# Optimization experiments

Measured on AMD Instinct MI355X. Metric: run time of the kernel, lower is better.

The kernel has to match this reference:

```python
import jax, jax.numpy as jnp
import numpy as np

E = 2048   # embed_dim
H = 16     # num query heads
D = E // H # head_dim = 128
B = 2
S = 2048


def setup_inputs() -> dict:
    key = jax.random.key(0)
    ks = jax.random.split(key, 12)
    sc = 0.02
    return {
        "input": jax.random.normal(ks[0], (B, S, E), jnp.float32),
        "kv": jax.random.normal(ks[1], (B, S, E), jnp.float32),
        "Wq": jax.random.normal(ks[2], (E, E), jnp.float32) * sc,
        "bq": jnp.zeros((E,), jnp.float32),
        "Wk": jax.random.normal(ks[3], (D, E), jnp.float32) * sc,
        "bk": jnp.zeros((D,), jnp.float32),
        "Wv": jax.random.normal(ks[4], (D, E), jnp.float32) * sc,
        "bv": jnp.zeros((D,), jnp.float32),
        "Wo": jax.random.normal(ks[5], (E, E), jnp.float32) * sc,
        "bo": jnp.zeros((E,), jnp.float32),
        "expanding_context": 0,
    }


def reference(input, kv, Wq, bq, Wk, bk, Wv, bv, Wo, bo, expanding_context):
    b, s, _ = input.shape
    # projections (torch Linear: x @ W.T + b)
    q = (input @ Wq.T + bq).reshape(b, s, H, D).transpose(0, 2, 1, 3)  # [B,H,S,D]
    k = kv @ Wk.T + bk  # [B,S,D] single KV head
    v = kv @ Wv.T + bv  # [B,S,D]
    # scores with single KV head broadcast across query heads
    scores = jnp.einsum('bhsd,btd->bhst', q, k) / jnp.sqrt(jnp.float32(D))
    causal = jnp.triu(jnp.ones((s, s), bool), k=1)  # True above diagonal
    scores = jnp.where(causal[None, None], jnp.float32(-jnp.inf), scores)
    attn = jax.nn.softmax(scores, axis=-1)
    out = jnp.einsum('bhst,btd->bhsd', attn, v)  # [B,H,S,D]
    out = out.transpose(0, 2, 1, 3).reshape(b, s, E)
    return out @ Wo.T + bo
```

## Files before the change

### kernel.cpp

```cpp
#include <hip/hip_runtime.h>

#define B_  2
#define S_  2048
#define E_  2048
#define H_  16
#define D_  128
#define BS_ (B_*S_)

typedef __bf16 bf16_t;
typedef __bf16 bf16x8 __attribute__((ext_vector_type(8)));
typedef __bf16 bf16x4 __attribute__((ext_vector_type(4)));
typedef float  f32x4  __attribute__((ext_vector_type(4)));

#define QSCALE 0.1275174131003543f

__device__ __forceinline__ void gld16(const bf16_t* g, bf16_t* l) {
    __builtin_amdgcn_global_load_lds(
        (const __attribute__((address_space(1))) void*)g,
        (__attribute__((address_space(3))) void*)l,
        16, 0, 0);
}

__global__ void cvt_all(const float* __restrict__ s0, const float* __restrict__ s1,
                        const float* __restrict__ s2, const float* __restrict__ s3,
                        const float* __restrict__ s4, const float* __restrict__ s5,
                        bf16_t* d0, bf16_t* d1, bf16_t* d2,
                        bf16_t* d3, bf16_t* d4, bf16_t* d5)
{
    long i = ((long)blockIdx.x * blockDim.x + threadIdx.x) * 4;
    const float* s; bf16_t* d;
    if      (i <  8388608) { s = s0; d = d0; }
    else if (i < 16777216) { s = s1; d = d1; i -=  8388608; }
    else if (i < 20971520) { s = s2; d = d2; i -= 16777216; }
    else if (i < 21233664) { s = s3; d = d3; i -= 20971520; }
    else if (i < 21495808) { s = s4; d = d4; i -= 21233664; }
    else                   { s = s5; d = d5; i -= 21495808; }
    float4 v = *(const float4*)(s + i);
    bf16x4 o;
    o[0] = (bf16_t)v.x; o[1] = (bf16_t)v.y; o[2] = (bf16_t)v.z; o[3] = (bf16_t)v.w;
    *(bf16x4*)(d + i) = o;
}

__device__ __forceinline__ void gemm_tile(
    const bf16_t* __restrict__ A, const bf16_t* __restrict__ W,
    const float* __restrict__ biasA, const float* __restrict__ biasB,
    float* __restrict__ Cf, bf16_t* __restrict__ Cb,
    int N, int K, float scale, int m0, int n0,
    bf16_t* As, bf16_t* Bs)
{
    const int tid  = threadIdx.x;
    const int wave = tid >> 6, lane = tid & 63;
    const int wm = wave >> 1, wn = wave & 1;
    const int lrow = lane & 15, quad = lane >> 4;
    const int r8 = lane >> 3, c8 = (lane & 7) << 3;

    f32x4 acc[4][4] = {};

    for (int k0 = 0; k0 < K; k0 += 64) {
        __syncthreads();
#pragma unroll
        for (int j = 0; j < 4; ++j) {
            int base = (wave * 4 + j) * 8;
            gld16(A + (size_t)(m0 + base + r8) * K + k0 + c8, &As[base * 64]);
            gld16(W + (size_t)(n0 + base + r8) * K + k0 + c8, &Bs[base * 64]);
        }
        __syncthreads();
#pragma unroll
        for (int ks = 0; ks < 2; ++ks) {
            bf16x8 af[4], bfr[4];
#pragma unroll
            for (int mt = 0; mt < 4; ++mt)
                af[mt] = *(const bf16x8*)&As[(wm * 64 + mt * 16 + lrow) * 64 + ks * 32 + quad * 8];
#pragma unroll
            for (int nt = 0; nt < 4; ++nt)
                bfr[nt] = *(const bf16x8*)&Bs[(wn * 64 + nt * 16 + lrow) * 64 + ks * 32 + quad * 8];
#pragma unroll
            for (int mt = 0; mt < 4; ++mt)
#pragma unroll
                for (int nt = 0; nt < 4; ++nt)
                    acc[mt][nt] = __builtin_amdgcn_mfma_f32_16x16x32_bf16(
                        af[mt], bfr[nt], acc[mt][nt], 0, 0, 0);
        }
    }

#pragma unroll
    for (int mt = 0; mt < 4; ++mt) {
#pragma unroll
        for (int nt = 0; nt < 4; ++nt) {
            int col = n0 + wn * 64 + nt * 16 + lrow;
            const float* bp = biasA; int ci = col;
            if (biasB && col >= 128) { bp = biasB; ci = col - 128; }
            float bv = bp[ci];
#pragma unroll
            for (int r = 0; r < 4; ++r) {
                int row = m0 + wm * 64 + mt * 16 + quad * 4 + r;
                float v = (acc[mt][nt][r] + bv) * scale;
                if (Cf) Cf[(size_t)row * N + col] = v;
                else    Cb[(size_t)row * N + col] = (bf16_t)v;
            }
        }
    }
}

__global__ __launch_bounds__(256) void gemm_qkv(
    const bf16_t* __restrict__ xb, const bf16_t* __restrict__ kvb,
    const bf16_t* __restrict__ Wq, const bf16_t* __restrict__ Wkv,
    const float* __restrict__ bq, const float* __restrict__ bk,
    const float* __restrict__ bv,
    bf16_t* __restrict__ Qb, bf16_t* __restrict__ KVb)
{
    __shared__ __align__(16) bf16_t As[128 * 64];
    __shared__ __align__(16) bf16_t Bs[128 * 64];
    const int m0 = blockIdx.y * 128;
    if (blockIdx.x < 16) {
        gemm_tile(xb, Wq, bq, nullptr, nullptr, Qb, E_, E_, QSCALE,
                  m0, blockIdx.x * 128, As, Bs);
    } else {
        gemm_tile(kvb, Wkv, bk, bv, nullptr, KVb, 256, E_, 1.0f,
                  m0, (blockIdx.x - 16) * 128, As, Bs);
    }
}

__global__ __launch_bounds__(256) void gemm_o(
    const bf16_t* __restrict__ A, const bf16_t* __restrict__ W,
    const float* __restrict__ bias, float* __restrict__ Cf)
{
    __shared__ __align__(16) bf16_t As[128 * 64];
    __shared__ __align__(16) bf16_t Bs[128 * 64];
    gemm_tile(A, W, bias, nullptr, Cf, nullptr, E_, E_, 1.0f,
              blockIdx.y * 128, blockIdx.x * 128, As, Bs);
}

__global__ __launch_bounds__(512, 4) void mqa_attn(
    const bf16_t* __restrict__ Q, const bf16_t* __restrict__ KV,
    bf16_t* __restrict__ O)
{
    __shared__ __align__(16) bf16_t Kt[64][136];
    __shared__ __align__(16) bf16_t Vt[128][72];
    __shared__ __align__(16) bf16_t Pl[8][16][72];

    const int bx = blockIdx.x, h = blockIdx.y, b = blockIdx.z;
    const int qb = b ? bx : (15 - bx);
    const int tid = threadIdx.x, wave = tid >> 6, lane = tid & 63;
    const int lrow = lane & 15, quad = lane >> 4;
    const int q0 = qb * 128 + wave * 16;

    const bf16_t* kvp = KV + (size_t)(b * S_) * 256;

    bf16x8 qf[4];
    {
        const bf16_t* qp = Q + ((size_t)(b * S_ + q0 + lrow)) * E_ + h * D_ + quad * 8;
#pragma unroll
        for (int ks = 0; ks < 4; ++ks) qf[ks] = *(const bf16x8*)(qp + ks * 32);
    }

    f32x4 oacc[8] = {};
    float rs[4] = {0.f, 0.f, 0.f, 0.f};

    const int ntiles = 2 * qb + 2;
    bf16x8 kreg[2], vreg[2];

#pragma unroll
    for (int i = 0; i < 2; ++i) {
        int c = tid + 512 * i;
        kreg[i] = *(const bf16x8*)(kvp + (size_t)(c >> 4) * 256 + ((c & 15) << 3));
        vreg[i] = *(const bf16x8*)(kvp + (size_t)(c & 63) * 256 + 128 + ((c >> 6) << 3));
    }

    for (int kt = 0; kt < ntiles; ++kt) {
        const int k_base = kt * 64;
        __syncthreads();
#pragma unroll
        for (int i = 0; i < 2; ++i) {
            int c = tid + 512 * i;
            *(bf16x8*)&Kt[c >> 4][(c & 15) << 3] = kreg[i];
            int n = c & 63, d0 = (c >> 6) << 3;
#pragma unroll
            for (int j = 0; j < 8; ++j) Vt[d0 + j][n] = vreg[i][j];
        }
        __syncthreads();
        if (kt + 1 < ntiles) {
            const int nb = (kt + 1) * 64;
#pragma unroll
            for (int i = 0; i < 2; ++i) {
                int c = tid + 512 * i;
                kreg[i] = *(const bf16x8*)(kvp + (size_t)(nb + (c >> 4)) * 256 + ((c & 15) << 3));
                vreg[i] = *(const bf16x8*)(kvp + (size_t)(nb + (c & 63)) * 256 + 128 + ((c >> 6) << 3));
            }
        }

        if (k_base <= q0 + 15) {
            f32x4 sc[4] = {};
#pragma unroll
            for (int ks = 0; ks < 4; ++ks) {
                bf16x8 a = qf[ks];
#pragma unroll
                for (int c = 0; c < 4; ++c) {
                    bf16x8 kb = *(const bf16x8*)&Kt[c * 16 + lrow][ks * 32 + quad * 8];
                    sc[c] = __builtin_amdgcn_mfma_f32_16x16x32_bf16(a, kb, sc[c], 0, 0, 0);
                }
            }
            const bool diag = (k_base + 63 > q0);
#pragma unroll
            for (int c = 0; c < 4; ++c) {
#pragma unroll
                for (int r = 0; r < 4; ++r) {
                    float s = sc[c][r];
                    if (diag) {
                        int kj = k_base + c * 16 + lrow;
                        int qi = q0 + quad * 4 + r;
                        if (kj > qi) s = -1e30f;
                    }
                    float p = exp2f(fminf(s, 110.f));
                    rs[r] += p;
                    Pl[wave][quad * 4 + r][c * 16 + lrow] = (bf16_t)p;
                }
            }
#pragma unroll
            for (int ks = 0; ks < 2; ++ks) {
                bf16x8 ap = *(const bf16x8*)&Pl[wave][lrow][ks * 32 + quad * 8];
#pragma unroll
                for (int dt = 0; dt < 8; ++dt) {
                    bf16x8 bv = *(const bf16x8*)&Vt[dt * 16 + lrow][ks * 32 + quad * 8];
                    oacc[dt] = __builtin_amdgcn_mfma_f32_16x16x32_bf16(ap, bv, oacc[dt], 0, 0, 0);
                }
            }
        }
    }

#pragma unroll
    for (int off = 8; off >= 1; off >>= 1)
#pragma unroll
        for (int r = 0; r < 4; ++r) rs[r] += __shfl_xor(rs[r], off, 16);
#pragma unroll
    for (int r = 0; r < 4; ++r) {
        float inv = 1.0f / rs[r];
        int row = q0 + quad * 4 + r;
#pragma unroll
        for (int dt = 0; dt < 8; ++dt)
            O[((size_t)(b * S_ + row)) * E_ + h * D_ + dt * 16 + lrow] =
                (bf16_t)(oacc[dt][r] * inv);
    }
}

extern "C" void kernel_launch(void* const* d_in, const int* in_sizes, int n_in,
                              void* d_out, int out_size, void* d_ws, size_t ws_size,
                              hipStream_t stream)
{
    const float* x   = (const float*)d_in[0];
    const float* kv  = (const float*)d_in[1];
    const float* Wq  = (const float*)d_in[2];
    const float* bq  = (const float*)d_in[3];
    const float* Wk  = (const float*)d_in[4];
    const float* bk  = (const float*)d_in[5];
    const float* Wv  = (const float*)d_in[6];
    const float* bv  = (const float*)d_in[7];
    const float* Wo  = (const float*)d_in[8];
    const float* bo  = (const float*)d_in[9];
    float* out = (float*)d_out;

    bf16_t* p    = (bf16_t*)d_ws;
    bf16_t* xb   = p;  p += (size_t)BS_ * E_;
    bf16_t* kvb  = p;  p += (size_t)BS_ * E_;
    bf16_t* Wqb  = p;  p += (size_t)E_ * E_;
    bf16_t* Wkvb = p;  p += (size_t)2 * D_ * E_;
    bf16_t* Wob  = p;  p += (size_t)E_ * E_;
    bf16_t* Qb   = p;  p += (size_t)BS_ * E_;
    bf16_t* KVb  = p;  p += (size_t)BS_ * 256;
    bf16_t* Ob   = p;  p += (size_t)BS_ * E_;

    cvt_all<<<dim3(25088), dim3(256), 0, stream>>>(
        x, kv, Wq, Wk, Wv, Wo,
        xb, kvb, Wqb, Wkvb, Wkvb + (size_t)D_ * E_, Wob);

    gemm_qkv<<<dim3(18, BS_ / 128), 256, 0, stream>>>(
        xb, kvb, Wqb, Wkvb, bq, bk, bv, Qb, KVb);

    mqa_attn<<<dim3(S_ / 128, H_, B_), 512, 0, stream>>>(Qb, KVb, Ob);

    gemm_o<<<dim3(E_ / 128, BS_ / 128), 256, 0, stream>>>(Ob, Wob, bo, out);
}
```

Baseline: 365.7 us.

## Fuse fp32 activation conversion into QKV GEMM with register-staged double buffering

Stops converting the x and kv activations to bf16 in a separate pass. The QKV GEMM now reads fp32 activations directly and converts them while staging tiles into LDS, and only the weights are still pre-converted. The GEMM tile loop is rewritten from global_load_lds with two barriers per step to a register-prefetched, double-buffered LDS pipeline with one barrier per step. This saves a full activation read/write pass, but doubles LDS per block and raises register pressure, and the QKV GEMM now reads fp32 A tiles, so it moves twice the bytes for them.

```diff
diff --git a/kernel.cpp b/kernel.cpp
--- a/kernel.cpp
+++ b/kernel.cpp
@@ -14,66 +14,110 @@
 
 #define QSCALE 0.1275174131003543f
 
-__device__ __forceinline__ void gld16(const bf16_t* g, bf16_t* l) {
-    __builtin_amdgcn_global_load_lds(
-        (const __attribute__((address_space(1))) void*)g,
-        (__attribute__((address_space(3))) void*)l,
-        16, 0, 0);
-}
-
-__global__ void cvt_all(const float* __restrict__ s0, const float* __restrict__ s1,
-                        const float* __restrict__ s2, const float* __restrict__ s3,
-                        const float* __restrict__ s4, const float* __restrict__ s5,
-                        bf16_t* d0, bf16_t* d1, bf16_t* d2,
-                        bf16_t* d3, bf16_t* d4, bf16_t* d5)
+__global__ void cvt_w(const float* __restrict__ s0, const float* __restrict__ s1,
+                      const float* __restrict__ s2, const float* __restrict__ s3,
+                      bf16_t* d0, bf16_t* d1, bf16_t* d2, bf16_t* d3)
 {
     long i = ((long)blockIdx.x * blockDim.x + threadIdx.x) * 4;
     const float* s; bf16_t* d;
-    if      (i <  8388608) { s = s0; d = d0; }
-    else if (i < 16777216) { s = s1; d = d1; i -=  8388608; }
-    else if (i < 20971520) { s = s2; d = d2; i -= 16777216; }
-    else if (i < 21233664) { s = s3; d = d3; i -= 20971520; }
-    else if (i < 21495808) { s = s4; d = d4; i -= 21233664; }
-    else                   { s = s5; d = d5; i -= 21495808; }
+    if      (i < 4194304) { s = s0; d = d0; }
+    else if (i < 4456448) { s = s1; d = d1; i -= 4194304; }
+    else if (i < 4718592) { s = s2; d = d2; i -= 4456448; }
+    else                  { s = s3; d = d3; i -= 4718592; }
     float4 v = *(const float4*)(s + i);
     bf16x4 o;
     o[0] = (bf16_t)v.x; o[1] = (bf16_t)v.y; o[2] = (bf16_t)v.z; o[3] = (bf16_t)v.w;
     *(bf16x4*)(d + i) = o;
 }
 
-__device__ __forceinline__ void gemm_tile(
-    const bf16_t* __restrict__ A, const bf16_t* __restrict__ W,
-    const float* __restrict__ biasA, const float* __restrict__ biasB,
+template<bool AF32>
+__device__ __forceinline__ void gemm_tile_db(
+    const void* Ap, const bf16_t* __restrict__ W,
+    const float* __restrict__ bias,
     float* __restrict__ Cf, bf16_t* __restrict__ Cb,
-    int N, int K, float scale, int m0, int n0,
+    int N, int K, float scale, int m0, int w_n0, int c_n0,
     bf16_t* As, bf16_t* Bs)
 {
     const int tid  = threadIdx.x;
     const int wave = tid >> 6, lane = tid & 63;
     const int wm = wave >> 1, wn = wave & 1;
     const int lrow = lane & 15, quad = lane >> 4;
-    const int r8 = lane >> 3, c8 = (lane & 7) << 3;
+
+    const float*  Af = (const float*)Ap;
+    const bf16_t* Ab = (const bf16_t*)Ap;
+
+    float4 arf[8];
+    uint4  arb[4];
+    uint4  brb[4];
+
+    auto loadA = [&](int k0) {
+        if constexpr (AF32) {
+#pragma unroll
+            for (int j = 0; j < 8; ++j) {
+                int c = tid + 256 * j, row = c >> 4, col = (c & 15) << 2;
+                arf[j] = *(const float4*)(Af + (size_t)(m0 + row) * K + k0 + col);
+            }
+        } else {
+#pragma unroll
+            for (int j = 0; j < 4; ++j) {
+                int c = tid + 256 * j, row = c >> 3, col = (c & 7) << 3;
+                arb[j] = *(const uint4*)(Ab + (size_t)(m0 + row) * K + k0 + col);
+            }
+        }
+    };
+    auto loadB = [&](int k0) {
+#pragma unroll
+        for (int j = 0; j < 4; ++j) {
+            int c = tid + 256 * j, row = c >> 3, col = (c & 7) << 3;
+            brb[j] = *(const uint4*)(W + (size_t)(w_n0 + row) * K + k0 + col);
+        }
+    };
+    auto storeA = [&](bf16_t* dst) {
+        if constexpr (AF32) {
+#pragma unroll
+            for (int j = 0; j < 8; ++j) {
+                int c = tid + 256 * j, row = c >> 4, col = (c & 15) << 2;
+                bf16x4 o;
+                o[0] = (bf16_t)arf[j].x; o[1] = (bf16_t)arf[j].y;
+                o[2] = (bf16_t)arf[j].z; o[3] = (bf16_t)arf[j].w;
+                *(bf16x4*)&dst[row * 64 + col] = o;
+            }
+        } else {
+#pragma unroll
+            for (int j = 0; j < 4; ++j) {
+                int c = tid + 256 * j, row = c >> 3, col = (c & 7) << 3;
+                *(uint4*)&dst[row * 64 + col] = arb[j];
+            }
+        }
+    };
+    auto storeB = [&](bf16_t* dst) {
+#pragma unroll
+        for (int j = 0; j < 4; ++j) {
+            int c = tid + 256 * j, row = c >> 3, col = (c & 7) << 3;
+            *(uint4*)&dst[row * 64 + col] = brb[j];
+        }
+    };
 
     f32x4 acc[4][4] = {};
 
+    loadA(0); loadB(0);
+    storeA(As); storeB(Bs);
+    loadA(64); loadB(64);
+
+    int cur = 0;
     for (int k0 = 0; k0 < K; k0 += 64) {
         __syncthreads();
-#pragma unroll
-        for (int j = 0; j < 4; ++j) {
-            int base = (wave * 4 + j) * 8;
-            gld16(A + (size_t)(m0 + base + r8) * K + k0 + c8, &As[base * 64]);
-            gld16(W + (size_t)(n0 + base + r8) * K + k0 + c8, &Bs[base * 64]);
-        }
-        __syncthreads();
+        const bf16_t* Ac = As + cur * 8192;
+        const bf16_t* Bc = Bs + cur * 8192;
 #pragma unroll
         for (int ks = 0; ks < 2; ++ks) {
             bf16x8 af[4], bfr[4];
 #pragma unroll
             for (int mt = 0; mt < 4; ++mt)
-                af[mt] = *(const bf16x8*)&As[(wm * 64 + mt * 16 + lrow) * 64 + ks * 32 + quad * 8];
+                af[mt] = *(const bf16x8*)&Ac[(wm * 64 + mt * 16 + lrow) * 64 + ks * 32 + quad * 8];
 #pragma unroll
             for (int nt = 0; nt < 4; ++nt)
-                bfr[nt] = *(const bf16x8*)&Bs[(wn * 64 + nt * 16 + lrow) * 64 + ks * 32 + quad * 8];
+                bfr[nt] = *(const bf16x8*)&Bc[(wn * 64 + nt * 16 + lrow) * 64 + ks * 32 + quad * 8];
 #pragma unroll
             for (int mt = 0; mt < 4; ++mt)
 #pragma unroll
@@ -81,20 +125,25 @@
                     acc[mt][nt] = __builtin_amdgcn_mfma_f32_16x16x32_bf16(
                         af[mt], bfr[nt], acc[mt][nt], 0, 0, 0);
         }
+        if (k0 + 64 < K) {
+            storeA(As + (cur ^ 1) * 8192);
+            storeB(Bs + (cur ^ 1) * 8192);
+            if (k0 + 128 < K) { loadA(k0 + 128); loadB(k0 + 128); }
+        }
+        cur ^= 1;
     }
 
 #pragma unroll
     for (int mt = 0; mt < 4; ++mt) {
 #pragma unroll
         for (int nt = 0; nt < 4; ++nt) {
-            int col = n0 + wn * 64 + nt * 16 + lrow;
-            const float* bp = biasA; int ci = col;
-            if (biasB && col >= 128) { bp = biasB; ci = col - 128; }
-            float bv = bp[ci];
+            int nn = wn * 64 + nt * 16 + lrow;
+            float bvv = bias[w_n0 + nn];
+            int col = c_n0 + nn;
 #pragma unroll
             for (int r = 0; r < 4; ++r) {
                 int row = m0 + wm * 64 + mt * 16 + quad * 4 + r;
-                float v = (acc[mt][nt][r] + bv) * scale;
+                float v = (acc[mt][nt][r] + bvv) * scale;
                 if (Cf) Cf[(size_t)row * N + col] = v;
                 else    Cb[(size_t)row * N + col] = (bf16_t)v;
             }
@@ -102,33 +151,36 @@
     }
 }
 
-__global__ __launch_bounds__(256) void gemm_qkv(
-    const bf16_t* __restrict__ xb, const bf16_t* __restrict__ kvb,
-    const bf16_t* __restrict__ Wq, const bf16_t* __restrict__ Wkv,
+__global__ __launch_bounds__(256, 2) void gemm_qkv(
+    const float* __restrict__ x, const float* __restrict__ kv,
+    const bf16_t* __restrict__ Wq, const bf16_t* __restrict__ Wk,
+    const bf16_t* __restrict__ Wv,
     const float* __restrict__ bq, const float* __restrict__ bk,
     const float* __restrict__ bv,
     bf16_t* __restrict__ Qb, bf16_t* __restrict__ KVb)
 {
-    __shared__ __align__(16) bf16_t As[128 * 64];
-    __shared__ __align__(16) bf16_t Bs[128 * 64];
+    __shared__ __align__(16) bf16_t As[2 * 8192];
+    __shared__ __align__(16) bf16_t Bs[2 * 8192];
     const int m0 = blockIdx.y * 128;
     if (blockIdx.x < 16) {
-        gemm_tile(xb, Wq, bq, nullptr, nullptr, Qb, E_, E_, QSCALE,
-                  m0, blockIdx.x * 128, As, Bs);
+        int n0 = blockIdx.x * 128;
+        gemm_tile_db<true>(x, Wq, bq, nullptr, Qb, E_, E_, QSCALE, m0, n0, n0, As, Bs);
+    } else if (blockIdx.x == 16) {
+        gemm_tile_db<true>(kv, Wk, bk, nullptr, KVb, 256, E_, 1.0f, m0, 0, 0, As, Bs);
     } else {
-        gemm_tile(kvb, Wkv, bk, bv, nullptr, KVb, 256, E_, 1.0f,
-                  m0, (blockIdx.x - 16) * 128, As, Bs);
-    }
-}
-
-__global__ __launch_bounds__(256) void gemm_o(
+        gemm_tile_db<true>(kv, Wv, bv, nullptr, KVb, 256, E_, 1.0f, m0, 0, 128, As, Bs);
+    }
+}
+
+__global__ __launch_bounds__(256, 2) void gemm_o(
     const bf16_t* __restrict__ A, const bf16_t* __restrict__ W,
     const float* __restrict__ bias, float* __restrict__ Cf)
 {
-    __shared__ __align__(16) bf16_t As[128 * 64];
-    __shared__ __align__(16) bf16_t Bs[128 * 64];
-    gemm_tile(A, W, bias, nullptr, Cf, nullptr, E_, E_, 1.0f,
-              blockIdx.y * 128, blockIdx.x * 128, As, Bs);
+    __shared__ __align__(16) bf16_t As[2 * 8192];
+    __shared__ __align__(16) bf16_t Bs[2 * 8192];
+    int n0 = blockIdx.x * 128;
+    gemm_tile_db<false>(A, W, bias, Cf, nullptr, E_, E_, 1.0f,
+                        blockIdx.y * 128, n0, n0, As, Bs);
 }
 
 __global__ __launch_bounds__(512, 4) void mqa_attn(
@@ -260,21 +312,19 @@
     float* out = (float*)d_out;
 
     bf16_t* p    = (bf16_t*)d_ws;
-    bf16_t* xb   = p;  p += (size_t)BS_ * E_;
-    bf16_t* kvb  = p;  p += (size_t)BS_ * E_;
     bf16_t* Wqb  = p;  p += (size_t)E_ * E_;
-    bf16_t* Wkvb = p;  p += (size_t)2 * D_ * E_;
+    bf16_t* Wkb  = p;  p += (size_t)D_ * E_;
+    bf16_t* Wvb  = p;  p += (size_t)D_ * E_;
     bf16_t* Wob  = p;  p += (size_t)E_ * E_;
     bf16_t* Qb   = p;  p += (size_t)BS_ * E_;
     bf16_t* KVb  = p;  p += (size_t)BS_ * 256;
     bf16_t* Ob   = p;  p += (size_t)BS_ * E_;
 
-    cvt_all<<<dim3(25088), dim3(256), 0, stream>>>(
-        x, kv, Wq, Wk, Wv, Wo,
-        xb, kvb, Wqb, Wkvb, Wkvb + (size_t)D_ * E_, Wob);
+    cvt_w<<<dim3(8704), dim3(256), 0, stream>>>(
+        Wq, Wk, Wv, Wo, Wqb, Wkb, Wvb, Wob);
 
     gemm_qkv<<<dim3(18, BS_ / 128), 256, 0, stream>>>(
-        xb, kvb, Wqb, Wkvb, bq, bk, bv, Qb, KVb);
+        x, kv, Wqb, Wkb, Wvb, bq, bk, bv, Qb, KVb);
 
     mqa_attn<<<dim3(S_ / 128, H_, B_), 512, 0, stream>>>(Qb, KVb, Ob);
 
```

Measured after the change: 495.0 us. +35.4%, slower.

## Split-K the Q and output projection GEMMs with fp32 atomic accumulation

Applied to the files above, without the earlier changes.

The Q projection and output projection GEMMs are split into two halves along K via a third grid dimension, with partial results combined by fp32 atomicAdd into zeroed buffers. The intent is to double the block count for these 512-tile GEMMs and fill more compute units. Q is now stored as fp32 and scaled and converted to bf16 inside the attention kernel, and the input buffer is reused for the attention output. This costs extra memsets, atomic traffic, doubled Q storage bandwidth, and an accumulation order that is no longer deterministic.

```diff
diff --git a/kernel.cpp b/kernel.cpp
--- a/kernel.cpp
+++ b/kernel.cpp
@@ -41,11 +41,12 @@
     *(bf16x4*)(d + i) = o;
 }
 
-__device__ __forceinline__ void gemm_tile(
+template<int EP>
+__device__ __forceinline__ void gemm_tile_sk(
     const bf16_t* __restrict__ A, const bf16_t* __restrict__ W,
     const float* __restrict__ biasA, const float* __restrict__ biasB,
     float* __restrict__ Cf, bf16_t* __restrict__ Cb,
-    int N, int K, float scale, int m0, int n0,
+    int N, int K, int kb, int ke, int m0, int w_n0, int c_n0, bool addb,
     bf16_t* As, bf16_t* Bs)
 {
     const int tid  = threadIdx.x;
@@ -56,13 +57,13 @@
 
     f32x4 acc[4][4] = {};
 
-    for (int k0 = 0; k0 < K; k0 += 64) {
+    for (int k0 = kb; k0 < ke; k0 += 64) {
         __syncthreads();
 #pragma unroll
         for (int j = 0; j < 4; ++j) {
             int base = (wave * 4 + j) * 8;
             gld16(A + (size_t)(m0 + base + r8) * K + k0 + c8, &As[base * 64]);
-            gld16(W + (size_t)(n0 + base + r8) * K + k0 + c8, &Bs[base * 64]);
+            gld16(W + (size_t)(w_n0 + base + r8) * K + k0 + c8, &Bs[base * 64]);
         }
         __syncthreads();
 #pragma unroll
@@ -87,16 +88,17 @@
     for (int mt = 0; mt < 4; ++mt) {
 #pragma unroll
         for (int nt = 0; nt < 4; ++nt) {
-            int col = n0 + wn * 64 + nt * 16 + lrow;
-            const float* bp = biasA; int ci = col;
-            if (biasB && col >= 128) { bp = biasB; ci = col - 128; }
-            float bv = bp[ci];
+            int nn = wn * 64 + nt * 16 + lrow;
+            int col = c_n0 + nn;
+            float bvv;
+            if (EP == 0) bvv = addb ? biasA[w_n0 + nn] : 0.0f;
+            else         bvv = (biasB && col >= 128) ? biasB[col - 128] : biasA[col];
 #pragma unroll
             for (int r = 0; r < 4; ++r) {
                 int row = m0 + wm * 64 + mt * 16 + quad * 4 + r;
-                float v = (acc[mt][nt][r] + bv) * scale;
-                if (Cf) Cf[(size_t)row * N + col] = v;
-                else    Cb[(size_t)row * N + col] = (bf16_t)v;
+                float v = acc[mt][nt][r] + bvv;
+                if (EP == 0) atomicAdd(&Cf[(size_t)row * N + col], v);
+                else         Cb[(size_t)row * N + col] = (bf16_t)v;
             }
         }
     }
@@ -107,17 +109,20 @@
     const bf16_t* __restrict__ Wq, const bf16_t* __restrict__ Wkv,
     const float* __restrict__ bq, const float* __restrict__ bk,
     const float* __restrict__ bv,
-    bf16_t* __restrict__ Qb, bf16_t* __restrict__ KVb)
-{
-    __shared__ __align__(16) bf16_t As[128 * 64];
-    __shared__ __align__(16) bf16_t Bs[128 * 64];
-    const int m0 = blockIdx.y * 128;
+    float* __restrict__ Qf, bf16_t* __restrict__ KVb)
+{
+    if (blockIdx.x >= 16 && blockIdx.z == 1) return;
+    __shared__ __align__(16) bf16_t As[8192];
+    __shared__ __align__(16) bf16_t Bs[8192];
+    const int m0 = blockIdx.y * 128, z = blockIdx.z;
     if (blockIdx.x < 16) {
-        gemm_tile(xb, Wq, bq, nullptr, nullptr, Qb, E_, E_, QSCALE,
-                  m0, blockIdx.x * 128, As, Bs);
+        int n0 = blockIdx.x * 128;
+        gemm_tile_sk<0>(xb, Wq, bq, nullptr, Qf, nullptr, E_, E_,
+                        z * 1024, z * 1024 + 1024, m0, n0, n0, z == 0, As, Bs);
     } else {
-        gemm_tile(kvb, Wkv, bk, bv, nullptr, KVb, 256, E_, 1.0f,
-                  m0, (blockIdx.x - 16) * 128, As, Bs);
+        int n0 = (blockIdx.x - 16) * 128;
+        gemm_tile_sk<1>(kvb, Wkv, bk, bv, nullptr, KVb, 256, E_,
+                        0, E_, m0, n0, n0, true, As, Bs);
     }
 }
 
@@ -125,14 +130,15 @@
     const bf16_t* __restrict__ A, const bf16_t* __restrict__ W,
     const float* __restrict__ bias, float* __restrict__ Cf)
 {
-    __shared__ __align__(16) bf16_t As[128 * 64];
-    __shared__ __align__(16) bf16_t Bs[128 * 64];
-    gemm_tile(A, W, bias, nullptr, Cf, nullptr, E_, E_, 1.0f,
-              blockIdx.y * 128, blockIdx.x * 128, As, Bs);
+    __shared__ __align__(16) bf16_t As[8192];
+    __shared__ __align__(16) bf16_t Bs[8192];
+    const int n0 = blockIdx.x * 128, z = blockIdx.z;
+    gemm_tile_sk<0>(A, W, bias, nullptr, Cf, nullptr, E_, E_,
+                    z * 1024, z * 1024 + 1024, blockIdx.y * 128, n0, n0, z == 0, As, Bs);
 }
 
 __global__ __launch_bounds__(512, 4) void mqa_attn(
-    const bf16_t* __restrict__ Q, const bf16_t* __restrict__ KV,
+    const float* __restrict__ Qf, const bf16_t* __restrict__ KV,
     bf16_t* __restrict__ O)
 {
     __shared__ __align__(16) bf16_t Kt[64][136];
@@ -149,9 +155,18 @@
 
     bf16x8 qf[4];
     {
-        const bf16_t* qp = Q + ((size_t)(b * S_ + q0 + lrow)) * E_ + h * D_ + quad * 8;
-#pragma unroll
-        for (int ks = 0; ks < 4; ++ks) qf[ks] = *(const bf16x8*)(qp + ks * 32);
+        const float* qp = Qf + ((size_t)(b * S_ + q0 + lrow)) * E_ + h * D_ + quad * 8;
+#pragma unroll
+        for (int ks = 0; ks < 4; ++ks) {
+            float4 a = *(const float4*)(qp + ks * 32);
+            float4 c = *(const float4*)(qp + ks * 32 + 4);
+            bf16x8 o;
+            o[0] = (bf16_t)(a.x * QSCALE); o[1] = (bf16_t)(a.y * QSCALE);
+            o[2] = (bf16_t)(a.z * QSCALE); o[3] = (bf16_t)(a.w * QSCALE);
+            o[4] = (bf16_t)(c.x * QSCALE); o[5] = (bf16_t)(c.y * QSCALE);
+            o[6] = (bf16_t)(c.z * QSCALE); o[7] = (bf16_t)(c.w * QSCALE);
+            qf[ks] = o;
+        }
     }
 
     f32x4 oacc[8] = {};
@@ -260,23 +275,25 @@
     float* out = (float*)d_out;
 
     bf16_t* p    = (bf16_t*)d_ws;
-    bf16_t* xb   = p;  p += (size_t)BS_ * E_;
+    bf16_t* slA  = p;  p += (size_t)BS_ * E_;
     bf16_t* kvb  = p;  p += (size_t)BS_ * E_;
     bf16_t* Wqb  = p;  p += (size_t)E_ * E_;
     bf16_t* Wkvb = p;  p += (size_t)2 * D_ * E_;
     bf16_t* Wob  = p;  p += (size_t)E_ * E_;
-    bf16_t* Qb   = p;  p += (size_t)BS_ * E_;
     bf16_t* KVb  = p;  p += (size_t)BS_ * 256;
-    bf16_t* Ob   = p;  p += (size_t)BS_ * E_;
+    float*  Qf   = (float*)p;
+
+    hipMemsetAsync(Qf, 0, (size_t)BS_ * E_ * 4, stream);
+    hipMemsetAsync(out, 0, (size_t)out_size * 4, stream);
 
     cvt_all<<<dim3(25088), dim3(256), 0, stream>>>(
         x, kv, Wq, Wk, Wv, Wo,
-        xb, kvb, Wqb, Wkvb, Wkvb + (size_t)D_ * E_, Wob);
-
-    gemm_qkv<<<dim3(18, BS_ / 128), 256, 0, stream>>>(
-        xb, kvb, Wqb, Wkvb, bq, bk, bv, Qb, KVb);
-
-    mqa_attn<<<dim3(S_ / 128, H_, B_), 512, 0, stream>>>(Qb, KVb, Ob);
-
-    gemm_o<<<dim3(E_ / 128, BS_ / 128), 256, 0, stream>>>(Ob, Wob, bo, out);
-}
+        slA, kvb, Wqb, Wkvb, Wkvb + (size_t)D_ * E_, Wob);
+
+    gemm_qkv<<<dim3(18, BS_ / 128, 2), 256, 0, stream>>>(
+        slA, kvb, Wqb, Wkvb, bq, bk, bv, Qf, KVb);
+
+    mqa_attn<<<dim3(S_ / 128, H_, B_), 512, 0, stream>>>(Qf, KVb, slA);
+
+    gemm_o<<<dim3(E_ / 128, BS_ / 128, 2), 256, 0, stream>>>(slA, Wob, bo, out);
+}
```

Result: slower. 445.2 us (+21.7%).

## Double-buffer GEMM LDS tiles to overlap global loads with MFMA

Applied to the files above, without the earlier changes.

Doubles the LDS buffers in the shared GEMM tile and issues the next K-slice's global-to-LDS loads before computing on the current slice, dropping one barrier per iteration. This is meant to hide global memory latency behind the matrix-core work in the QKV and output projections. The epilogue is also templated so the fp32/bf16 store choice and bias selection resolve at compile time. LDS use per block doubles to 64 KB, which can reduce occupancy.

```diff
diff --git a/kernel.cpp b/kernel.cpp
--- a/kernel.cpp
+++ b/kernel.cpp
@@ -41,11 +41,12 @@
     *(bf16x4*)(d + i) = o;
 }
 
+template<int EP>
 __device__ __forceinline__ void gemm_tile(
     const bf16_t* __restrict__ A, const bf16_t* __restrict__ W,
     const float* __restrict__ biasA, const float* __restrict__ biasB,
     float* __restrict__ Cf, bf16_t* __restrict__ Cb,
-    int N, int K, float scale, int m0, int n0,
+    int N, int K, float scale, int m0, int w_n0, int c_n0,
     bf16_t* As, bf16_t* Bs)
 {
     const int tid  = threadIdx.x;
@@ -56,24 +57,33 @@
 
     f32x4 acc[4][4] = {};
 
-    for (int k0 = 0; k0 < K; k0 += 64) {
-        __syncthreads();
+    auto stage = [&](int k0, int buf) {
 #pragma unroll
         for (int j = 0; j < 4; ++j) {
             int base = (wave * 4 + j) * 8;
-            gld16(A + (size_t)(m0 + base + r8) * K + k0 + c8, &As[base * 64]);
-            gld16(W + (size_t)(n0 + base + r8) * K + k0 + c8, &Bs[base * 64]);
-        }
+            gld16(A + (size_t)(m0 + base + r8) * K + k0 + c8,
+                  &As[buf * 8192 + base * 64]);
+            gld16(W + (size_t)(w_n0 + base + r8) * K + k0 + c8,
+                  &Bs[buf * 8192 + base * 64]);
+        }
+    };
+
+    stage(0, 0);
+    const int nk = K >> 6;
+    for (int ki = 0; ki < nk; ++ki) {
         __syncthreads();
+        if (ki + 1 < nk) stage((ki + 1) << 6, (ki + 1) & 1);
+        const bf16_t* Ac = As + (ki & 1) * 8192;
+        const bf16_t* Bc = Bs + (ki & 1) * 8192;
 #pragma unroll
         for (int ks = 0; ks < 2; ++ks) {
             bf16x8 af[4], bfr[4];
 #pragma unroll
             for (int mt = 0; mt < 4; ++mt)
-                af[mt] = *(const bf16x8*)&As[(wm * 64 + mt * 16 + lrow) * 64 + ks * 32 + quad * 8];
+                af[mt] = *(const bf16x8*)&Ac[(wm * 64 + mt * 16 + lrow) * 64 + ks * 32 + quad * 8];
 #pragma unroll
             for (int nt = 0; nt < 4; ++nt)
-                bfr[nt] = *(const bf16x8*)&Bs[(wn * 64 + nt * 16 + lrow) * 64 + ks * 32 + quad * 8];
+                bfr[nt] = *(const bf16x8*)&Bc[(wn * 64 + nt * 16 + lrow) * 64 + ks * 32 + quad * 8];
 #pragma unroll
             for (int mt = 0; mt < 4; ++mt)
 #pragma unroll
@@ -87,16 +97,16 @@
     for (int mt = 0; mt < 4; ++mt) {
 #pragma unroll
         for (int nt = 0; nt < 4; ++nt) {
-            int col = n0 + wn * 64 + nt * 16 + lrow;
-            const float* bp = biasA; int ci = col;
-            if (biasB && col >= 128) { bp = biasB; ci = col - 128; }
-            float bv = bp[ci];
+            int nn = wn * 64 + nt * 16 + lrow;
+            int col = c_n0 + nn;
+            float bvv = (EP == 1 && biasB && col >= 128) ? biasB[col - 128]
+                                                         : biasA[EP == 1 ? col : w_n0 + nn];
 #pragma unroll
             for (int r = 0; r < 4; ++r) {
                 int row = m0 + wm * 64 + mt * 16 + quad * 4 + r;
-                float v = (acc[mt][nt][r] + bv) * scale;
-                if (Cf) Cf[(size_t)row * N + col] = v;
-                else    Cb[(size_t)row * N + col] = (bf16_t)v;
+                float v = (acc[mt][nt][r] + bvv) * scale;
+                if (EP == 0) Cf[(size_t)row * N + col] = v;
+                else         Cb[(size_t)row * N + col] = (bf16_t)v;
             }
         }
     }
@@ -109,15 +119,17 @@
     const float* __restrict__ bv,
     bf16_t* __restrict__ Qb, bf16_t* __restrict__ KVb)
 {
-    __shared__ __align__(16) bf16_t As[128 * 64];
-    __shared__ __align__(16) bf16_t Bs[128 * 64];
+    __shared__ __align__(16) bf16_t As[2 * 8192];
+    __shared__ __align__(16) bf16_t Bs[2 * 8192];
     const int m0 = blockIdx.y * 128;
     if (blockIdx.x < 16) {
-        gemm_tile(xb, Wq, bq, nullptr, nullptr, Qb, E_, E_, QSCALE,
-                  m0, blockIdx.x * 128, As, Bs);
+        int n0 = blockIdx.x * 128;
+        gemm_tile<1>(xb, Wq, bq, nullptr, nullptr, Qb, E_, E_, QSCALE,
+                     m0, n0, n0, As, Bs);
     } else {
-        gemm_tile(kvb, Wkv, bk, bv, nullptr, KVb, 256, E_, 1.0f,
-                  m0, (blockIdx.x - 16) * 128, As, Bs);
+        int n0 = (blockIdx.x - 16) * 128;
+        gemm_tile<1>(kvb, Wkv, bk, bv, nullptr, KVb, 256, E_, 1.0f,
+                     m0, n0, n0, As, Bs);
     }
 }
 
@@ -125,10 +137,11 @@
     const bf16_t* __restrict__ A, const bf16_t* __restrict__ W,
     const float* __restrict__ bias, float* __restrict__ Cf)
 {
-    __shared__ __align__(16) bf16_t As[128 * 64];
-    __shared__ __align__(16) bf16_t Bs[128 * 64];
-    gemm_tile(A, W, bias, nullptr, Cf, nullptr, E_, E_, 1.0f,
-              blockIdx.y * 128, blockIdx.x * 128, As, Bs);
+    __shared__ __align__(16) bf16_t As[2 * 8192];
+    __shared__ __align__(16) bf16_t Bs[2 * 8192];
+    int n0 = blockIdx.x * 128;
+    gemm_tile<0>(A, W, bias, nullptr, Cf, nullptr, E_, E_, 1.0f,
+                 blockIdx.y * 128, n0, n0, As, Bs);
 }
 
 __global__ __launch_bounds__(512, 4) void mqa_attn(
```

Result: no change. 365.4 us (-0.1%).
